# Optimization experiments

Hardware: AMD Instinct MI355X
Metric: run time of the kernel (lower is better)

The kernel has to match this reference:

```python
import jax, jax.numpy as jnp
import numpy as np

EPS = 1e-5

def _bn(x, g, b):
    # training-mode BatchNorm1d over the batch axis (axis 0), biased variance
    m = jnp.mean(x, axis=0)
    v = jnp.var(x, axis=0)
    return g * (x - m) / jnp.sqrt(v + EPS) + b

def _mlp(x, w1, b1, g1, be1, w2, b2, g2, be2, w3, b3):
    # Linear -> BN -> ReLU -> Linear -> BN -> ReLU -> Linear
    x = jax.nn.relu(_bn(x @ w1.T + b1, g1, be1))
    x = jax.nn.relu(_bn(x @ w2.T + b2, g2, be2))
    return x @ w3.T + b3

def setup_inputs() -> dict:
    key = jax.random.key(0)
    ks = jax.random.split(key, 10)
    B, S, D = 256, 512, 128
    w = lambda k: jax.random.normal(k, (D, D), jnp.float32) * 0.05
    return {
        "s": jax.random.normal(ks[0], (B, S, D), jnp.float32),
        "c": jax.random.normal(ks[1], (B, D), jnp.float32),
        "s_w1": w(ks[2]), "s_b1": jnp.zeros((D,), jnp.float32),
        "s_g1": jnp.ones((D,), jnp.float32), "s_be1": jnp.zeros((D,), jnp.float32),
        "s_w2": w(ks[3]), "s_b2": jnp.zeros((D,), jnp.float32),
        "s_g2": jnp.ones((D,), jnp.float32), "s_be2": jnp.zeros((D,), jnp.float32),
        "s_w3": w(ks[4]), "s_b3": jnp.zeros((D,), jnp.float32),
        "c_w1": w(ks[5]), "c_b1": jnp.zeros((D,), jnp.float32),
        "c_g1": jnp.ones((D,), jnp.float32), "c_be1": jnp.zeros((D,), jnp.float32),
        "c_w2": w(ks[6]), "c_b2": jnp.zeros((D,), jnp.float32),
        "c_g2": jnp.ones((D,), jnp.float32), "c_be2": jnp.zeros((D,), jnp.float32),
        "c_w3": w(ks[7]), "c_b3": jnp.zeros((D,), jnp.float32),
    }

def reference(s, c,
              s_w1, s_b1, s_g1, s_be1, s_w2, s_b2, s_g2, s_be2, s_w3, s_b3,
              c_w1, c_b1, c_g1, c_be1, c_w2, c_b2, c_g2, c_be2, c_w3, c_b3):
    # c_mlp: [B, D] -> [B, D] (BN over batch)
    c_out = _mlp(c, c_w1, c_b1, c_g1, c_be1, c_w2, c_b2, c_g2, c_be2, c_w3, c_b3)
    # s_mlp applied per sequence slice; BN stats over batch axis 0 only
    # (matches the torch loop where each s[:, i, :] gets its own BN stats).
    # s: [B, S, D]; _bn with axis=0 gives per-(slice, feature) stats.
    s_h = _mlp(s, s_w1, s_b1, s_g1, s_be1, s_w2, s_b2, s_g2, s_be2, s_w3, s_b3)
    s_out = s_h * c_out[:, None, :]          # context gate, [B, S, D]
    aggregated_c = jnp.max(s_out, axis=1)    # pooling == 'max', [B, D]
    return (s_out, aggregated_c)
```

## Files before the change

kernel.cpp:

```cpp
#include <hip/hip_runtime.h>
#include <hip/hip_bf16.h>

#define BATCH 256
#define SEQ   512
#define DIM   128
#define LDSK  136

typedef __attribute__((ext_vector_type(8))) __bf16  bf16x8;
typedef __attribute__((ext_vector_type(4))) __bf16  bf16x4;
typedef __attribute__((ext_vector_type(4))) float   f32x4;

template<int RT>
__device__ __forceinline__ void matmul_layer(
    const __bf16* __restrict__ Xa, const __bf16* __restrict__ wg,
    const float* __restrict__ bias, f32x4 (&acc)[RT][8], int wave, int m, int q)
{
  const int rowbase = wave * RT * 16;
#pragma unroll
  for (int ct = 0; ct < 8; ++ct) {
    const float b = bias[ct * 16 + m];
    const f32x4 bv = {b, b, b, b};
#pragma unroll
    for (int rt = 0; rt < RT; ++rt) acc[rt][ct] = bv;
  }
#pragma unroll
  for (int ks = 0; ks < 4; ++ks) {
    const int k0 = ks * 32 + q * 8;
    bf16x8 a[RT], bw[8];
#pragma unroll
    for (int rt = 0; rt < RT; ++rt)
      a[rt] = *(const bf16x8*)(Xa + (rowbase + rt * 16 + m) * LDSK + k0);
#pragma unroll
    for (int ct = 0; ct < 8; ++ct)
      bw[ct] = *(const bf16x8*)(wg + (ct * 16 + m) * DIM + k0);
#pragma unroll
    for (int rt = 0; rt < RT; ++rt)
#pragma unroll
      for (int ct = 0; ct < 8; ++ct)
        acc[rt][ct] = __builtin_amdgcn_mfma_f32_16x16x32_bf16(a[rt], bw[ct], acc[rt][ct], 0, 0, 0);
  }
}

template<int RT>
__device__ __forceinline__ void stats_accum(
    const f32x4 (&acc)[RT][8], float* sumA, float* sqA, int m, int q)
{
#pragma unroll
  for (int ct = 0; ct < 8; ++ct) {
    float s = 0.f, ss = 0.f;
#pragma unroll
    for (int rt = 0; rt < RT; ++rt)
#pragma unroll
      for (int r = 0; r < 4; ++r) { const float v = acc[rt][ct][r]; s += v; ss += v * v; }
    s  += __shfl_xor(s, 16, 64);  s  += __shfl_xor(s, 32, 64);
    ss += __shfl_xor(ss, 16, 64); ss += __shfl_xor(ss, 32, 64);
    if (q == 0) { atomicAdd(&sumA[ct * 16 + m], s); atomicAdd(&sqA[ct * 16 + m], ss); }
  }
}

__device__ __forceinline__ void bn_coefs(int tid, const float* __restrict__ g,
    const float* __restrict__ be, float* sumA, float* sqA, float* cA, float* cC)
{
  if (tid < DIM) {
    const float mean = sumA[tid] * (1.0f / BATCH);
    const float var  = sqA[tid]  * (1.0f / BATCH) - mean * mean;
    const float rstd = rsqrtf(var + 1e-5f);
    const float a = g[tid] * rstd;
    cA[tid] = a;
    cC[tid] = be[tid] - a * mean;
    sumA[tid] = 0.f; sqA[tid] = 0.f;
  }
}

template<int RT>
__device__ __forceinline__ void bn_relu_store(
    const f32x4 (&acc)[RT][8], __bf16* Xa, const float* cA, const float* cC,
    int wave, int m, int q)
{
  const int rowbase = wave * RT * 16;
#pragma unroll
  for (int ct = 0; ct < 8; ++ct) {
    const int n = ct * 16 + m;
    const float a = cA[n], c = cC[n];
#pragma unroll
    for (int rt = 0; rt < RT; ++rt)
#pragma unroll
      for (int r = 0; r < 4; ++r) {
        const float y = fmaxf(0.f, a * acc[rt][ct][r] + c);
        const int row = rowbase + rt * 16 + q * 4 + r;
        Xa[row * LDSK + n] = (__bf16)y;
      }
  }
}

template<int NW, bool GATE>
__global__ __launch_bounds__(NW * 64, 2)
void mlp_kernel(const float* __restrict__ xin, long xrow_stride,
                const __bf16* __restrict__ w1, const __bf16* __restrict__ w2,
                const __bf16* __restrict__ w3,
                const float* __restrict__ b1, const float* __restrict__ g1, const float* __restrict__ be1,
                const float* __restrict__ b2, const float* __restrict__ g2, const float* __restrict__ be2,
                const float* __restrict__ b3,
                const float* __restrict__ gate,
                float* __restrict__ out)
{
  const int tid  = threadIdx.x;
  constexpr int NT = NW * 64;
  constexpr int RT = 16 / NW;
  const int wave = tid >> 6, lane = tid & 63;
  const int m = lane & 15, q = lane >> 4;
  const int slice = GATE ? blockIdx.x : 0;
  const float* x0 = GATE ? (xin + (long)slice * DIM) : xin;

  __shared__ __bf16 Xa[BATCH * LDSK];
  __shared__ float sumA[DIM], sqA[DIM], cA[DIM], cC[DIM];

  for (int t = tid; t < DIM; t += NT) { sumA[t] = 0.f; sqA[t] = 0.f; }

  {
    const int rpi = NT / 32;
    const int r0  = tid >> 5;
    const int c4  = (tid & 31) * 4;
#pragma unroll
    for (int it = 0; it < BATCH / rpi; ++it) {
      const int r = it * rpi + r0;
      const float4 v = *(const float4*)(x0 + (long)r * xrow_stride + c4);
      bf16x4 h = { (__bf16)v.x, (__bf16)v.y, (__bf16)v.z, (__bf16)v.w };
      *(bf16x4*)(Xa + r * LDSK + c4) = h;
    }
  }
  __syncthreads();

  f32x4 acc[RT][8];

  matmul_layer<RT>(Xa, w1, b1, acc, wave, m, q);
  stats_accum<RT>(acc, sumA, sqA, m, q);
  __syncthreads();
  bn_coefs(tid, g1, be1, sumA, sqA, cA, cC);
  __syncthreads();
  bn_relu_store<RT>(acc, Xa, cA, cC, wave, m, q);
  __syncthreads();

  matmul_layer<RT>(Xa, w2, b2, acc, wave, m, q);
  stats_accum<RT>(acc, sumA, sqA, m, q);
  __syncthreads();
  bn_coefs(tid, g2, be2, sumA, sqA, cA, cC);
  __syncthreads();
  bn_relu_store<RT>(acc, Xa, cA, cC, wave, m, q);
  __syncthreads();

  matmul_layer<RT>(Xa, w3, b3, acc, wave, m, q);

  const int rowbase = wave * RT * 16;
#pragma unroll
  for (int ct = 0; ct < 8; ++ct) {
    const int col = ct * 16 + m;
#pragma unroll
    for (int rt = 0; rt < RT; ++rt) {
#pragma unroll
      for (int r = 0; r < 4; ++r) {
        const int row = rowbase + rt * 16 + q * 4 + r;
        float y = acc[rt][ct][r];
        if (GATE) {
          y *= gate[row * DIM + col];
          out[((long)row * SEQ + slice) * DIM + col] = y;
        } else {
          out[row * DIM + col] = y;
        }
      }
    }
  }
}

__global__ void prep_kernel(const float* __restrict__ w0, const float* __restrict__ w1,
                            const float* __restrict__ w2, const float* __restrict__ w3,
                            const float* __restrict__ w4, const float* __restrict__ w5,
                            __bf16* __restrict__ dst)
{
  const int idx = blockIdx.x * blockDim.x + threadIdx.x;
  const int mi  = idx >> 12;
  const int j   = (idx & 4095) * 4;
  const float* srcs[6] = {w0, w1, w2, w3, w4, w5};
  const float4 v = *(const float4*)(srcs[mi] + j);
  bf16x4 h = { (__bf16)v.x, (__bf16)v.y, (__bf16)v.z, (__bf16)v.w };
  *(bf16x4*)(dst + mi * 16384 + j) = h;
}

__global__ __launch_bounds__(512) void maxpool_kernel(
    const float* __restrict__ sout, float* __restrict__ agg)
{
  __shared__ float red[512];
  const int b = blockIdx.x;
  const int t = threadIdx.x;
  const int d = t & 127, ig = t >> 7;
  const float* p = sout + (long)b * SEQ * DIM + d;
  float m0 = -INFINITY, m1 = -INFINITY, m2 = -INFINITY, m3 = -INFINITY;
  const int i0 = ig * 128;
#pragma unroll 8
  for (int i = i0; i < i0 + 128; i += 4) {
    m0 = fmaxf(m0, p[(long)(i + 0) * DIM]);
    m1 = fmaxf(m1, p[(long)(i + 1) * DIM]);
    m2 = fmaxf(m2, p[(long)(i + 2) * DIM]);
    m3 = fmaxf(m3, p[(long)(i + 3) * DIM]);
  }
  red[t] = fmaxf(fmaxf(m0, m1), fmaxf(m2, m3));
  __syncthreads();
  if (t < 128) {
    const float a = fmaxf(fmaxf(red[t], red[t + 128]), fmaxf(red[t + 256], red[t + 384]));
    agg[b * DIM + t] = a;
  }
}

extern "C" void kernel_launch(void* const* d_in, const int* in_sizes, int n_in,
                              void* d_out, int out_size, void* d_ws, size_t ws_size,
                              hipStream_t stream)
{
  const float* s     = (const float*)d_in[0];
  const float* c     = (const float*)d_in[1];
  const float* s_w1  = (const float*)d_in[2];
  const float* s_b1  = (const float*)d_in[3];
  const float* s_g1  = (const float*)d_in[4];
  const float* s_be1 = (const float*)d_in[5];
  const float* s_w2  = (const float*)d_in[6];
  const float* s_b2  = (const float*)d_in[7];
  const float* s_g2  = (const float*)d_in[8];
  const float* s_be2 = (const float*)d_in[9];
  const float* s_w3  = (const float*)d_in[10];
  const float* s_b3  = (const float*)d_in[11];
  const float* c_w1  = (const float*)d_in[12];
  const float* c_b1  = (const float*)d_in[13];
  const float* c_g1  = (const float*)d_in[14];
  const float* c_be1 = (const float*)d_in[15];
  const float* c_w2  = (const float*)d_in[16];
  const float* c_b2  = (const float*)d_in[17];
  const float* c_g2  = (const float*)d_in[18];
  const float* c_be2 = (const float*)d_in[19];
  const float* c_w3  = (const float*)d_in[20];
  const float* c_b3  = (const float*)d_in[21];

  float* out   = (float*)d_out;
  float* c_out = (float*)d_ws;
  __bf16* wbf  = (__bf16*)((char*)d_ws + (size_t)BATCH * DIM * sizeof(float));

  prep_kernel<<<96, 256, 0, stream>>>(s_w1, s_w2, s_w3, c_w1, c_w2, c_w3, wbf);

  mlp_kernel<8, false><<<1, 512, 0, stream>>>(
      c, (long)DIM,
      wbf + 3 * 16384, wbf + 4 * 16384, wbf + 5 * 16384,
      c_b1, c_g1, c_be1, c_b2, c_g2, c_be2, c_b3,
      nullptr, c_out);

  mlp_kernel<4, true><<<SEQ, 256, 0, stream>>>(
      s, (long)SEQ * DIM,
      wbf, wbf + 16384, wbf + 2 * 16384,
      s_b1, s_g1, s_be1, s_b2, s_g2, s_be2, s_b3,
      c_out, out);

  maxpool_kernel<<<BATCH, 512, 0, stream>>>(out, out + (long)BATCH * SEQ * DIM);
}
```

Measured before the change: 228.9 us.

## Stage gated MLP output through LDS for coalesced stores and vectorize maxpool

The final layer's accumulators are written into LDS as fp32 one row-tile at a time, then read back as float4 rows, multiplied by the gate, and stored to global memory. This replaces the strided scalar stores. The s-MLP now launches 8 waves per block instead of 4. The maxpool kernel uses 1024 threads with float4 loads and an LDS reduction. The cost is extra barriers and LDS round-trips, plus possible register pressure from the new launch bounds.

```diff
diff --git a/kernel.cpp b/kernel.cpp
--- a/kernel.cpp
+++ b/kernel.cpp
@@ -1,10 +1,12 @@
 #include <hip/hip_runtime.h>
 #include <hip/hip_bf16.h>
+#include <math.h>
 
 #define BATCH 256
 #define SEQ   512
 #define DIM   128
 #define LDSK  136
+#define LDSF  132
 
 typedef __attribute__((ext_vector_type(8))) __bf16  bf16x8;
 typedef __attribute__((ext_vector_type(4))) __bf16  bf16x4;
@@ -94,7 +96,7 @@
 }
 
 template<int NW, bool GATE>
-__global__ __launch_bounds__(NW * 64, 2)
+__global__ __launch_bounds__(NW * 64, NW / 2)
 void mlp_kernel(const float* __restrict__ xin, long xrow_stride,
                 const __bf16* __restrict__ w1, const __bf16* __restrict__ w2,
                 const __bf16* __restrict__ w3,
@@ -112,7 +114,8 @@
   const int slice = GATE ? blockIdx.x : 0;
   const float* x0 = GATE ? (xin + (long)slice * DIM) : xin;
 
-  __shared__ __bf16 Xa[BATCH * LDSK];
+  __shared__ __align__(16) char XaRaw[BATCH * LDSK * 2];
+  __bf16* Xa = (__bf16*)XaRaw;
   __shared__ float sumA[DIM], sqA[DIM], cA[DIM], cC[DIM];
 
   for (int t = tid; t < DIM; t += NT) { sumA[t] = 0.f; sqA[t] = 0.f; }
@@ -151,21 +154,41 @@
 
   matmul_layer<RT>(Xa, w3, b3, acc, wave, m, q);
 
-  const int rowbase = wave * RT * 16;
-#pragma unroll
-  for (int ct = 0; ct < 8; ++ct) {
-    const int col = ct * 16 + m;
+  if constexpr (GATE) {
+    float* Xf = (float*)XaRaw;
+    const int c4 = (tid & 31) * 4;
+    const int r0 = tid >> 5;
+    __syncthreads();
 #pragma unroll
     for (int rt = 0; rt < RT; ++rt) {
 #pragma unroll
-      for (int r = 0; r < 4; ++r) {
-        const int row = rowbase + rt * 16 + q * 4 + r;
-        float y = acc[rt][ct][r];
-        if (GATE) {
-          y *= gate[row * DIM + col];
-          out[((long)row * SEQ + slice) * DIM + col] = y;
-        } else {
-          out[row * DIM + col] = y;
+      for (int ct = 0; ct < 8; ++ct)
+#pragma unroll
+        for (int r = 0; r < 4; ++r)
+          Xf[(wave * 16 + q * 4 + r) * LDSF + ct * 16 + m] = acc[rt][ct][r];
+      __syncthreads();
+#pragma unroll
+      for (int it = 0; it < 8; ++it) {
+        const int crow = it * 16 + r0;
+        const int grow = (crow >> 4) * 32 + rt * 16 + (crow & 15);
+        float4 y = *(const float4*)(Xf + crow * LDSF + c4);
+        const float4 gv = *(const float4*)(gate + grow * DIM + c4);
+        y.x *= gv.x; y.y *= gv.y; y.z *= gv.z; y.w *= gv.w;
+        *(float4*)(out + ((long)grow * SEQ + slice) * DIM + c4) = y;
+      }
+      if (rt + 1 < RT) __syncthreads();
+    }
+  } else {
+    const int rowbase = wave * RT * 16;
+#pragma unroll
+    for (int ct = 0; ct < 8; ++ct) {
+      const int col = ct * 16 + m;
+#pragma unroll
+      for (int rt = 0; rt < RT; ++rt) {
+#pragma unroll
+        for (int r = 0; r < 4; ++r) {
+          const int row = rowbase + rt * 16 + q * 4 + r;
+          out[row * DIM + col] = acc[rt][ct][r];
         }
       }
     }
@@ -186,28 +209,32 @@
   *(bf16x4*)(dst + mi * 16384 + j) = h;
 }
 
-__global__ __launch_bounds__(512) void maxpool_kernel(
+__global__ __launch_bounds__(1024) void maxpool_kernel(
     const float* __restrict__ sout, float* __restrict__ agg)
 {
-  __shared__ float red[512];
+  __shared__ float4 red[1024];
   const int b = blockIdx.x;
   const int t = threadIdx.x;
-  const int d = t & 127, ig = t >> 7;
-  const float* p = sout + (long)b * SEQ * DIM + d;
-  float m0 = -INFINITY, m1 = -INFINITY, m2 = -INFINITY, m3 = -INFINITY;
-  const int i0 = ig * 128;
-#pragma unroll 8
-  for (int i = i0; i < i0 + 128; i += 4) {
-    m0 = fmaxf(m0, p[(long)(i + 0) * DIM]);
-    m1 = fmaxf(m1, p[(long)(i + 1) * DIM]);
-    m2 = fmaxf(m2, p[(long)(i + 2) * DIM]);
-    m3 = fmaxf(m3, p[(long)(i + 3) * DIM]);
-  }
-  red[t] = fmaxf(fmaxf(m0, m1), fmaxf(m2, m3));
-  __syncthreads();
-  if (t < 128) {
-    const float a = fmaxf(fmaxf(red[t], red[t + 128]), fmaxf(red[t + 256], red[t + 384]));
-    agg[b * DIM + t] = a;
+  const int c4 = (t & 31) * 4, rg = t >> 5;
+  const float* p = sout + (long)b * SEQ * DIM + c4;
+  float4 mx = {-INFINITY, -INFINITY, -INFINITY, -INFINITY};
+#pragma unroll 4
+  for (int i = rg; i < SEQ; i += 32) {
+    const float4 v = *(const float4*)(p + (long)i * DIM);
+    mx.x = fmaxf(mx.x, v.x); mx.y = fmaxf(mx.y, v.y);
+    mx.z = fmaxf(mx.z, v.z); mx.w = fmaxf(mx.w, v.w);
+  }
+  red[t] = mx;
+  __syncthreads();
+  if (t < 32) {
+    float4 a = red[t];
+#pragma unroll
+    for (int k = 1; k < 32; ++k) {
+      const float4 v = red[t + 32 * k];
+      a.x = fmaxf(a.x, v.x); a.y = fmaxf(a.y, v.y);
+      a.z = fmaxf(a.z, v.z); a.w = fmaxf(a.w, v.w);
+    }
+    *(float4*)(agg + b * DIM + c4) = a;
   }
 }
 
@@ -250,11 +277,11 @@
       c_b1, c_g1, c_be1, c_b2, c_g2, c_be2, c_b3,
       nullptr, c_out);
 
-  mlp_kernel<4, true><<<SEQ, 256, 0, stream>>>(
+  mlp_kernel<8, true><<<SEQ, 512, 0, stream>>>(
       s, (long)SEQ * DIM,
       wbf, wbf + 16384, wbf + 2 * 16384,
       s_b1, s_g1, s_be1, s_b2, s_g2, s_be2, s_b3,
       c_out, out);
 
-  maxpool_kernel<<<BATCH, 512, 0, stream>>>(out, out + (long)BATCH * SEQ * DIM);
-}
+  maxpool_kernel<<<BATCH, 1024, 0, stream>>>(out, out + (long)BATCH * SEQ * DIM);
+}
```

Result: slower. 269.2 us (+17.6%).
